# Kernel optimization log

Hardware: AMD Instinct MI355X
Metric: run time of the kernel (lower is better)

## Reference

```python
import jax, jax.numpy as jnp
import numpy as np

N = 50000   # nodes
E = 800000  # edges
B = 512     # graphs
EPS = 1e-5  # BatchNorm eps


def _p(k, shape, scale=0.05):
    return jax.random.normal(k, shape, dtype=jnp.float32) * scale


def setup_inputs() -> dict:
    key = jax.random.key(0)
    ks = jax.random.split(key, 24)
    inp = {
        "x": jax.random.normal(ks[0], (N, 4), dtype=jnp.float32),
        "edge_index": jax.random.randint(ks[1], (2, E), 0, N, dtype=jnp.int64),
        "edge_weight": jax.random.uniform(ks[2], (E,), dtype=jnp.float32),
        "batch": jnp.sort(jax.random.randint(ks[3], (N,), 0, B, dtype=jnp.int64)),
        # block1: GCNConv(4,64) + BN + shortcut Linear(4,64)
        "W1": _p(ks[4], (4, 64)), "b1": jnp.zeros((64,), jnp.float32),
        "g1": jnp.ones((64,), jnp.float32), "be1": jnp.zeros((64,), jnp.float32),
        "sW1": _p(ks[5], (4, 64)), "sb1": jnp.zeros((64,), jnp.float32),
        # block2: GCNConv(64,64) + BN, identity shortcut
        "W2": _p(ks[6], (64, 64)), "b2": jnp.zeros((64,), jnp.float32),
        "g2": jnp.ones((64,), jnp.float32), "be2": jnp.zeros((64,), jnp.float32),
        # block3: GCNConv(64,128) + BN + shortcut Linear(64,128)
        "W3": _p(ks[7], (64, 128)), "b3": jnp.zeros((128,), jnp.float32),
        "g3": jnp.ones((128,), jnp.float32), "be3": jnp.zeros((128,), jnp.float32),
        "sW3": _p(ks[8], (64, 128)), "sb3": jnp.zeros((128,), jnp.float32),
        # head: Linear(256,128) + BN + ReLU + Linear(128,1)
        "fW1": _p(ks[9], (256, 128)), "fb1": jnp.zeros((128,), jnp.float32),
        "fg": jnp.ones((128,), jnp.float32), "fbe": jnp.zeros((128,), jnp.float32),
        "fW2": _p(ks[10], (128, 1)), "fb2": jnp.zeros((1,), jnp.float32),
    }
    return inp


def _bn(x, g, b):
    # training-mode BatchNorm1d over node dim (biased variance)
    m = x.mean(0)
    v = x.var(0)
    return (x - m) * jax.lax.rsqrt(v + EPS) * g + b


def _gcn(x, W, b, src, dst, w, n):
    # PyG GCNConv: add self-loops (weight 1), symmetric normalization
    h = x @ W  # [n, out]
    loop = jnp.arange(n)
    s = jnp.concatenate([src, loop])
    d = jnp.concatenate([dst, loop])
    ww = jnp.concatenate([w, jnp.ones((n,), x.dtype)])
    deg = jax.ops.segment_sum(ww, d, num_segments=n)
    dis = jnp.where(deg > 0, jax.lax.rsqrt(jnp.maximum(deg, EPS)), 0.0)
    norm = dis[s] * ww * dis[d]  # [E+n]
    return jax.ops.segment_sum(h[s] * norm[:, None], d, num_segments=n) + b


def _block(x, W, b, g, be, sW, sb, src, dst, w, n):
    out = jax.nn.relu(_bn(_gcn(x, W, b, src, dst, w, n), g, be))
    sc = x if sW is None else x @ sW + sb
    return out + sc


def reference(x, edge_index, edge_weight, batch,
              W1, b1, g1, be1, sW1, sb1,
              W2, b2, g2, be2,
              W3, b3, g3, be3, sW3, sb3,
              fW1, fb1, fg, fbe, fW2, fb2):
    n = x.shape[0]
    src, dst = edge_index[0], edge_index[1]
    h = _block(x, W1, b1, g1, be1, sW1, sb1, src, dst, edge_weight, n)
    h = _block(h, W2, b2, g2, be2, None, None, src, dst, edge_weight, n)
    h = _block(h, W3, b3, g3, be3, sW3, sb3, src, dst, edge_weight, n)
    # global mean / max pooling per graph
    cnt = jax.ops.segment_sum(jnp.ones((n,), h.dtype), batch, num_segments=B)
    p1 = jax.ops.segment_sum(h, batch, num_segments=B) / jnp.maximum(cnt, 1.0)[:, None]
    p2 = jax.ops.segment_max(h, batch, num_segments=B)
    z = jnp.concatenate([p1, p2], axis=1)  # [B, 256]
    z = jax.nn.relu(_bn(z @ fW1 + fb1, fg, fbe))  # Dropout eval = identity
    return z @ fW2 + fb2  # [B, 1]
```

## Files before the change

### kernel.cpp

```cpp
#include <hip/hip_runtime.h>

#define BNEPS 1e-5f


__global__ void k_fill(float* p, int n, float v){
  int i = blockIdx.x*blockDim.x + threadIdx.x;
  if(i < n) p[i] = v;
}


__global__ void k_count(int* cnt, const int* __restrict__ dst, int E){
  int e = blockIdx.x*blockDim.x + threadIdx.x;
  if(e < E) atomicAdd(&cnt[dst[e]], 1);
}

__global__ void k_scan1(int* cnt, int* rowptr, int* bsum, int n){
  __shared__ int sh[256];
  int tid = threadIdx.x;
  int i = blockIdx.x*256 + tid;
  int v = (i < n) ? cnt[i] : 0;
  sh[tid] = v;
  __syncthreads();
  for(int o = 1; o < 256; o <<= 1){
    int t = (tid >= o) ? sh[tid-o] : 0;
    __syncthreads();
    sh[tid] += t;
    __syncthreads();
  }
  if(i < n){ rowptr[i] = sh[tid] - v; cnt[i] = 0; }
  if(tid == 255) bsum[blockIdx.x] = sh[255];
}

__global__ void k_scan2(int* bsum, int m){
  __shared__ int sh[256];
  int tid = threadIdx.x;
  int v = (tid < m) ? bsum[tid] : 0;
  sh[tid] = v;
  __syncthreads();
  for(int o = 1; o < 256; o <<= 1){
    int t = (tid >= o) ? sh[tid-o] : 0;
    __syncthreads();
    sh[tid] += t;
    __syncthreads();
  }
  if(tid < m) bsum[tid] = sh[tid] - v;
}

__global__ void k_scan3(int* rowptr, const int* bsum, int n, int E){
  int i = blockIdx.x*blockDim.x + threadIdx.x;
  if(i < n) rowptr[i] += bsum[i >> 8];
  if(i == 0) rowptr[n] = E;
}

__global__ void k_scatter2(const int* __restrict__ src, const int* __restrict__ dst,
                           const float* __restrict__ w, const int* __restrict__ rowptr,
                           int* cur, int2* __restrict__ erec, int E){
  int e = blockIdx.x*blockDim.x + threadIdx.x;
  if(e >= E) return;
  int d = dst[e];
  int idx = rowptr[d] + atomicAdd(&cur[d], 1);
  erec[idx] = make_int2(src[e], __float_as_int(w[e]));
}

__global__ void k_degdis(const int2* __restrict__ erec, const int* __restrict__ rowptr,
                         float* __restrict__ dis, int n){
  int i = blockIdx.x*blockDim.x + threadIdx.x;
  if(i >= n) return;
  float s = 1.0f;
  int e0 = rowptr[i], e1 = rowptr[i+1];
  for(int j = e0; j < e1; j++) s += __int_as_float(erec[j].y);
  dis[i] = rsqrtf(s);
}

__global__ void k_mknorm(int2* __restrict__ erec, const int* __restrict__ rowptr,
                         const float* __restrict__ dis, int n){
  int i = blockIdx.x*blockDim.x + threadIdx.x;
  if(i >= n) return;
  float di = dis[i];
  int e0 = rowptr[i], e1 = rowptr[i+1];
  for(int j = e0; j < e1; j++){
    int2 r = erec[j];
    erec[j].y = __float_as_int(dis[r.x] * __int_as_float(r.y) * di);
  }
}


__global__ __launch_bounds__(256)
void k_gcn1_fused(const float* __restrict__ X, const float* __restrict__ dis,
                  const int* __restrict__ rowptr, const int2* __restrict__ erec,
                  const float* __restrict__ W, const float* __restrict__ bias,
                  float* __restrict__ H, float* __restrict__ stats, int n){
  const int tid = threadIdx.x;
  const int lane = tid & 63;
  const int wid = tid >> 6;
  const int eg = lane >> 2;
  const int ch = lane & 3;
  const float w0 = W[lane], w1 = W[64+lane], w2 = W[128+lane], w3 = W[192+lane];
  const float bc = bias[lane];
  float s = 0.f, s2 = 0.f;
  for(int i = blockIdx.x*4 + wid; i < n; i += gridDim.x*4){
    int e0 = rowptr[i], e1 = rowptr[i+1];
    float acc = 0.f;
    for(int j = e0 + eg; j < e1; j += 16){
      int2 r = erec[j];
      acc += X[(size_t)r.x*4 + ch] * __int_as_float(r.y);
    }
    if(eg == 0){
      float d = dis[i];
      acc += X[(size_t)i*4 + ch] * d * d;
    }
    acc += __shfl_xor(acc, 4);
    acc += __shfl_xor(acc, 8);
    acc += __shfl_xor(acc, 16);
    acc += __shfl_xor(acc, 32);
    float p0 = __shfl(acc, 0), p1 = __shfl(acc, 1);
    float p2 = __shfl(acc, 2), p3 = __shfl(acc, 3);
    float h = bc + p0*w0 + p1*w1 + p2*w2 + p3*w3;
    H[(size_t)i*64 + lane] = h;
    s += h; s2 += h*h;
  }
  __shared__ float rs[256], rs2[256];
  rs[tid] = s; rs2[tid] = s2;
  __syncthreads();
  if(tid < 64){
    atomicAdd(&stats[tid],    rs[tid]+rs[tid+64]+rs[tid+128]+rs[tid+192]);
    atomicAdd(&stats[64+tid], rs2[tid]+rs2[tid+64]+rs2[tid+128]+rs2[tid+192]);
  }
}


template<int C>
__global__ void k_gather(const float* __restrict__ H, const float* __restrict__ dis,
                         const int* __restrict__ rowptr, const int2* __restrict__ erec,
                         float* __restrict__ P, int n){
  const int NPB = 256 / C;
  int i = blockIdx.x*NPB + threadIdx.x / C;
  int c = threadIdx.x % C;
  if(i >= n) return;
  float di = dis[i];
  float acc = H[(size_t)i*C + c]*di*di;
  int e0 = rowptr[i], e1 = rowptr[i+1];
  int j = e0;
  for(; j + 8 <= e1; j += 8){
    int2 r0 = erec[j],   r1 = erec[j+1], r2 = erec[j+2], r3 = erec[j+3];
    int2 r4 = erec[j+4], r5 = erec[j+5], r6 = erec[j+6], r7 = erec[j+7];
    float h0 = H[(size_t)r0.x*C + c];
    float h1 = H[(size_t)r1.x*C + c];
    float h2 = H[(size_t)r2.x*C + c];
    float h3 = H[(size_t)r3.x*C + c];
    float h4 = H[(size_t)r4.x*C + c];
    float h5 = H[(size_t)r5.x*C + c];
    float h6 = H[(size_t)r6.x*C + c];
    float h7 = H[(size_t)r7.x*C + c];
    acc += h0*__int_as_float(r0.y) + h1*__int_as_float(r1.y)
         + h2*__int_as_float(r2.y) + h3*__int_as_float(r3.y)
         + h4*__int_as_float(r4.y) + h5*__int_as_float(r5.y)
         + h6*__int_as_float(r6.y) + h7*__int_as_float(r7.y);
  }
  for(; j < e1; j++){
    int2 r = erec[j];
    acc += H[(size_t)r.x*C + c] * __int_as_float(r.y);
  }
  P[(size_t)i*C + c] = acc;
}


template<int C>
__global__ __launch_bounds__(256)
void k_gemm_tile(const float* __restrict__ X, const float* __restrict__ W,
                 const float* __restrict__ bias, float* __restrict__ H,
                 float* __restrict__ stats, int n, int ntiles){
  const int RR = C/16;
  const int CG = C/4;
  __shared__ float Xs[64*65];
  __shared__ float Ws[64*C];
  __shared__ float sst[2*C];
  const int tid = threadIdx.x;
  const int cg = tid % CG, rg = tid / CG;
  const int c0 = cg*4;
  for(int t = tid; t < 16*C; t += 256)
    reinterpret_cast<float4*>(Ws)[t] = reinterpret_cast<const float4*>(W)[t];
  const float4 bc = *reinterpret_cast<const float4*>(bias + c0);
  float sacc[4] = {0,0,0,0}, qacc[4] = {0,0,0,0};
  const float4* X4 = reinterpret_cast<const float4*>(X);
  for(int tile = blockIdx.x; tile < ntiles; tile += gridDim.x){
    const int r0 = tile*64;
    __syncthreads();
    #pragma unroll
    for(int q = 0; q < 4; q++){
      int idx = tid + q*256;
      int row = idx >> 4, k4 = idx & 15;
      float4 v = (r0+row < n) ? X4[(size_t)(r0+row)*16 + k4] : make_float4(0.f,0.f,0.f,0.f);
      Xs[(4*k4+0)*65 + row] = v.x;
      Xs[(4*k4+1)*65 + row] = v.y;
      Xs[(4*k4+2)*65 + row] = v.z;
      Xs[(4*k4+3)*65 + row] = v.w;
    }
    __syncthreads();
    float acc[RR][4];
    #pragma unroll
    for(int r = 0; r < RR; r++){ acc[r][0]=bc.x; acc[r][1]=bc.y; acc[r][2]=bc.z; acc[r][3]=bc.w; }
    #pragma unroll 8
    for(int k = 0; k < 64; k++){
      float4 wv = reinterpret_cast<const float4*>(Ws)[k*CG + cg];
      #pragma unroll
      for(int r = 0; r < RR; r++){
        float xv = Xs[k*65 + rg*RR + r];
        acc[r][0] = fmaf(xv, wv.x, acc[r][0]);
        acc[r][1] = fmaf(xv, wv.y, acc[r][1]);
        acc[r][2] = fmaf(xv, wv.z, acc[r][2]);
        acc[r][3] = fmaf(xv, wv.w, acc[r][3]);
      }
    }
    #pragma unroll
    for(int r = 0; r < RR; r++){
      int row = r0 + rg*RR + r;
      if(row < n){
        *reinterpret_cast<float4*>(H + (size_t)row*C + c0) =
            make_float4(acc[r][0], acc[r][1], acc[r][2], acc[r][3]);
        #pragma unroll
        for(int j = 0; j < 4; j++){ sacc[j] += acc[r][j]; qacc[j] += acc[r][j]*acc[r][j]; }
      }
    }
  }
  for(int t = tid; t < 2*C; t += 256) sst[t] = 0.f;
  __syncthreads();
  #pragma unroll
  for(int j = 0; j < 4; j++){
    atomicAdd(&sst[c0+j], sacc[j]);
    atomicAdd(&sst[C+c0+j], qacc[j]);
  }
  __syncthreads();
  for(int t = tid; t < 2*C; t += 256) atomicAdd(&stats[t], sst[t]);
}

template<int C>
__global__ __launch_bounds__(256)
void k_gemm_bnsc_tile(const float* __restrict__ X, const float* __restrict__ sW,
                      const float* __restrict__ sb,
                      const float* __restrict__ agg, const float* __restrict__ stats,
                      const float* __restrict__ g, const float* __restrict__ be,
                      float* __restrict__ out, int n, int ntiles){
  const int RR = C/16;
  const int CG = C/4;
  __shared__ float Xs[64*65];
  __shared__ float Ws[64*C];
  const int tid = threadIdx.x;
  const int cg = tid % CG, rg = tid / CG;
  const int c0 = cg*4;
  for(int t = tid; t < 16*C; t += 256)
    reinterpret_cast<float4*>(Ws)[t] = reinterpret_cast<const float4*>(sW)[t];
  const float4 bc = *reinterpret_cast<const float4*>(sb + c0);
  float scal[4], shft[4];
  {
    float invn = 1.0f / n;
    #pragma unroll
    for(int j = 0; j < 4; j++){
      float m = stats[c0+j]*invn;
      float v = stats[C+c0+j]*invn - m*m;
      float rs = rsqrtf(v + BNEPS) * g[c0+j];
      scal[j] = rs;
      shft[j] = be[c0+j] - m*rs;
    }
  }
  const float4* X4 = reinterpret_cast<const float4*>(X);
  for(int tile = blockIdx.x; tile < ntiles; tile += gridDim.x){
    const int r0 = tile*64;
    __syncthreads();
    #pragma unroll
    for(int q = 0; q < 4; q++){
      int idx = tid + q*256;
      int row = idx >> 4, k4 = idx & 15;
      float4 v = (r0+row < n) ? X4[(size_t)(r0+row)*16 + k4] : make_float4(0.f,0.f,0.f,0.f);
      Xs[(4*k4+0)*65 + row] = v.x;
      Xs[(4*k4+1)*65 + row] = v.y;
      Xs[(4*k4+2)*65 + row] = v.z;
      Xs[(4*k4+3)*65 + row] = v.w;
    }
    __syncthreads();
    float acc[RR][4];
    #pragma unroll
    for(int r = 0; r < RR; r++){ acc[r][0]=bc.x; acc[r][1]=bc.y; acc[r][2]=bc.z; acc[r][3]=bc.w; }
    #pragma unroll 8
    for(int k = 0; k < 64; k++){
      float4 wv = reinterpret_cast<const float4*>(Ws)[k*CG + cg];
      #pragma unroll
      for(int r = 0; r < RR; r++){
        float xv = Xs[k*65 + rg*RR + r];
        acc[r][0] = fmaf(xv, wv.x, acc[r][0]);
        acc[r][1] = fmaf(xv, wv.y, acc[r][1]);
        acc[r][2] = fmaf(xv, wv.z, acc[r][2]);
        acc[r][3] = fmaf(xv, wv.w, acc[r][3]);
      }
    }
    #pragma unroll
    for(int r = 0; r < RR; r++){
      int row = r0 + rg*RR + r;
      if(row < n){
        float4 a = *reinterpret_cast<const float4*>(agg + (size_t)row*C + c0);
        float4 o;
        o.x = fmaxf(a.x*scal[0] + shft[0], 0.f) + acc[r][0];
        o.y = fmaxf(a.y*scal[1] + shft[1], 0.f) + acc[r][1];
        o.z = fmaxf(a.z*scal[2] + shft[2], 0.f) + acc[r][2];
        o.w = fmaxf(a.w*scal[3] + shft[3], 0.f) + acc[r][3];
        *reinterpret_cast<float4*>(out + (size_t)row*C + c0) = o;
      }
    }
  }
}


template<int C>
__global__ void k_bn_add4(const float* __restrict__ agg, const float* __restrict__ stats,
                          const float* __restrict__ g, const float* __restrict__ be,
                          const float* __restrict__ add, float* __restrict__ out, int n){
  int idx = blockIdx.x*blockDim.x + threadIdx.x;
  if(idx >= n*(C/4)) return;
  int c = (idx % (C/4))*4;
  float invn = 1.0f / n;
  float4 sm = *reinterpret_cast<const float4*>(stats + c);
  float4 sq = *reinterpret_cast<const float4*>(stats + C + c);
  float4 g4 = *reinterpret_cast<const float4*>(g + c);
  float4 b4 = *reinterpret_cast<const float4*>(be + c);
  float4 a  = reinterpret_cast<const float4*>(agg)[idx];
  float4 ad = reinterpret_cast<const float4*>(add)[idx];
  float4 o;
  #define BN1(X) { float m = sm.X*invn; float v = sq.X*invn - m*m; \
    o.X = fmaxf((a.X-m)*rsqrtf(v+BNEPS)*g4.X + b4.X, 0.f) + ad.X; }
  BN1(x) BN1(y) BN1(z) BN1(w)
  #undef BN1
  reinterpret_cast<float4*>(out)[idx] = o;
}

__global__ void k_bn_sc4_v4(const float* __restrict__ agg, const float* __restrict__ stats,
                            const float* __restrict__ g, const float* __restrict__ be,
                            const float* __restrict__ X, const float* __restrict__ sW,
                            const float* __restrict__ sb, float* __restrict__ out, int n){
  int idx = blockIdx.x*blockDim.x + threadIdx.x;
  if(idx >= n*16) return;
  int i = idx >> 4;
  int c = (idx & 15)*4;
  float invn = 1.0f / n;
  float4 xr = *reinterpret_cast<const float4*>(X + (size_t)i*4);
  float4 s0 = *reinterpret_cast<const float4*>(sW + c);
  float4 s1 = *reinterpret_cast<const float4*>(sW + 64 + c);
  float4 s2 = *reinterpret_cast<const float4*>(sW + 128 + c);
  float4 s3 = *reinterpret_cast<const float4*>(sW + 192 + c);
  float4 sb4 = *reinterpret_cast<const float4*>(sb + c);
  float4 sm = *reinterpret_cast<const float4*>(stats + c);
  float4 sq = *reinterpret_cast<const float4*>(stats + 64 + c);
  float4 g4 = *reinterpret_cast<const float4*>(g + c);
  float4 b4 = *reinterpret_cast<const float4*>(be + c);
  float4 a  = reinterpret_cast<const float4*>(agg)[idx];
  float4 o;
  #define BN1(X) { float sc = xr.x*s0.X + xr.y*s1.X + xr.z*s2.X + xr.w*s3.X + sb4.X; \
    float m = sm.X*invn; float v = sq.X*invn - m*m; \
    o.X = fmaxf((a.X-m)*rsqrtf(v+BNEPS)*g4.X + b4.X, 0.f) + sc; }
  BN1(x) BN1(y) BN1(z) BN1(w)
  #undef BN1
  reinterpret_cast<float4*>(out)[idx] = o;
}


__global__ void k_pool(const float* __restrict__ H, const int* __restrict__ batch,
                       float* __restrict__ z, int n){
  int b = blockIdx.x, c = threadIdx.x;
  int lo = 0, hi = n;
  while(lo < hi){ int mid = (lo+hi)>>1; if(batch[mid] <  b) lo = mid+1; else hi = mid; }
  int start = lo;
  hi = n;
  while(lo < hi){ int mid = (lo+hi)>>1; if(batch[mid] <  b+1) lo = mid+1; else hi = mid; }
  int end = lo;
  float s = 0.f, mx = -INFINITY;
  for(int i = start; i < end; i++){
    float v = H[(size_t)i*128 + c];
    s += v; mx = fmaxf(mx, v);
  }
  int cnt = end - start;
  z[b*256 + c]       = s / fmaxf((float)cnt, 1.f);
  z[b*256 + 128 + c] = mx;
}

__global__ void k_head1(const float* __restrict__ z, const float* __restrict__ fW1,
                        const float* __restrict__ fb1, float* __restrict__ zr,
                        float* __restrict__ stats, int B){
  int idx = blockIdx.x*blockDim.x + threadIdx.x;
  int tid = threadIdx.x;
  float acc = 0.f;
  if(idx < B*128){
    int b = idx >> 7, c = idx & 127;
    acc = fb1[c];
    #pragma unroll 4
    for(int k = 0; k < 256; k++) acc = fmaf(z[b*256+k], fW1[k*128+c], acc);
    zr[idx] = acc;
  }
  __shared__ float rs[256], rs2[256];
  rs[tid] = acc; rs2[tid] = acc*acc;
  __syncthreads();
  if(tid < 128){
    atomicAdd(&stats[tid],     rs[tid]+rs[tid+128]);
    atomicAdd(&stats[128+tid], rs2[tid]+rs2[tid+128]);
  }
}

__global__ void k_final(const float* __restrict__ zr, const float* __restrict__ stats,
                        const float* __restrict__ fg, const float* __restrict__ fbe,
                        const float* __restrict__ fW2, const float* __restrict__ fb2,
                        float* __restrict__ out, int B){
  __shared__ float red[128];
  int b = blockIdx.x, c = threadIdx.x;
  float invn = 1.0f / B;
  float m  = stats[c]*invn;
  float v  = stats[128+c]*invn - m*m;
  float rs = rsqrtf(v + BNEPS);
  float val = fmaxf((zr[b*128+c]-m)*rs*fg[c] + fbe[c], 0.f) * fW2[c];
  red[c] = val;
  __syncthreads();
  for(int s = 64; s > 0; s >>= 1){
    if(c < s) red[c] += red[c+s];
    __syncthreads();
  }
  if(c == 0) out[b] = red[0] + fb2[0];
}


extern "C" void kernel_launch(void* const* d_in, const int* in_sizes, int n_in,
                              void* d_out, int out_size, void* d_ws, size_t ws_size,
                              hipStream_t stream){
  const float* x   = (const float*)d_in[0];
  const int*   ei  = (const int*)  d_in[1];
  const float* ew  = (const float*)d_in[2];
  const int*   bat = (const int*)  d_in[3];
  const float* W1  = (const float*)d_in[4];  const float* b1  = (const float*)d_in[5];
  const float* g1  = (const float*)d_in[6];  const float* be1 = (const float*)d_in[7];
  const float* sW1 = (const float*)d_in[8];  const float* sb1 = (const float*)d_in[9];
  const float* W2  = (const float*)d_in[10]; const float* b2  = (const float*)d_in[11];
  const float* g2  = (const float*)d_in[12]; const float* be2 = (const float*)d_in[13];
  const float* W3  = (const float*)d_in[14]; const float* b3  = (const float*)d_in[15];
  const float* g3  = (const float*)d_in[16]; const float* be3 = (const float*)d_in[17];
  const float* sW3 = (const float*)d_in[18]; const float* sb3 = (const float*)d_in[19];
  const float* fW1 = (const float*)d_in[20]; const float* fb1 = (const float*)d_in[21];
  const float* fg  = (const float*)d_in[22]; const float* fbe = (const float*)d_in[23];
  const float* fW2 = (const float*)d_in[24]; const float* fb2 = (const float*)d_in[25];
  float* out = (float*)d_out;

  const int n = in_sizes[0] / 4;
  const int E = in_sizes[2];
  const int B = out_size;
  const int* src = ei;
  const int* dst = ei + E;

  auto GB = [](long long t){ return (int)((t + 255) / 256); };
  const int nscanb = (n + 255) / 256;
  const int ntiles = (n + 63) / 64;

  float* ws = (float*)d_ws;
  size_t off = 0;
  auto alloc = [&](size_t cnt)->float*{ float* p = ws + off; off += (cnt + 63) & ~size_t(63); return p; };

  const size_t npad = ((size_t)n + 63) & ~size_t(63);
  float* bufA  = alloc((size_t)n * 64);
  float* hbuf  = alloc((size_t)n * 128);
  float* agg   = alloc((size_t)n * 128);
  float* z     = alloc((size_t)B * 256);
  float* zr    = alloc((size_t)B * 128);
  float* zreg  = alloc(npad + 1024);
  int*   cnt   = (int*)zreg;
  float* st1 = zreg + npad; float* st2 = st1 + 256;
  float* st3 = st2 + 256;   float* stH = st3 + 256;
  float* dis    = alloc(n);
  int*   rowptr = (int*)alloc(n + 1);
  int*   bsum   = (int*)alloc(256);
  int2*  erec   = (int2*)alloc((size_t)E * 2);

  k_fill<<<GB(npad + 1024),256,0,stream>>>(zreg, (int)(npad + 1024), 0.f);
  k_count<<<GB(E),256,0,stream>>>(cnt, dst, E);
  k_scan1<<<nscanb,256,0,stream>>>(cnt, rowptr, bsum, n);
  k_scan2<<<1,256,0,stream>>>(bsum, nscanb);
  k_scan3<<<GB(n),256,0,stream>>>(rowptr, bsum, n, E);
  k_scatter2<<<GB(E),256,0,stream>>>(src, dst, ew, rowptr, cnt, erec, E);
  k_degdis<<<GB(n),256,0,stream>>>(erec, rowptr, dis, n);
  k_mknorm<<<GB(n),256,0,stream>>>(erec, rowptr, dis, n);

  float* P = hbuf;
  k_gcn1_fused<<<512,256,0,stream>>>(x, dis, rowptr, erec, W1, b1, agg, st1, n);
  k_bn_sc4_v4<<<GB((long long)n*16),256,0,stream>>>(agg, st1, g1, be1, x, sW1, sb1, bufA, n);

  k_gather<64><<<(n+3)/4,256,0,stream>>>(bufA, dis, rowptr, erec, P, n);
  k_gemm_tile<64><<<512,256,0,stream>>>(P, W2, b2, agg, st2, n, ntiles);
  k_bn_add4<64><<<GB((long long)n*16),256,0,stream>>>(agg, st2, g2, be2, bufA, bufA, n);

  k_gather<64><<<(n+3)/4,256,0,stream>>>(bufA, dis, rowptr, erec, P, n);
  k_gemm_tile<128><<<512,256,0,stream>>>(P, W3, b3, agg, st3, n, ntiles);
  k_gemm_bnsc_tile<128><<<512,256,0,stream>>>(bufA, sW3, sb3, agg, st3, g3, be3, hbuf, n, ntiles);

  k_pool<<<B,128,0,stream>>>(hbuf, bat, z, n);
  k_head1<<<GB((long long)B*128),256,0,stream>>>(z, fW1, fb1, zr, stH, B);
  k_final<<<B,128,0,stream>>>(zr, stH, fg, fbe, fW2, fb2, out, B);
}
```

Measured before the change: 487.5 us.

## Store 64-wide node features in fp16 and reuse atomic ranks for CSR scatter

The 64-channel intermediate feature buffer is now stored as half precision, and the gather, BN-add, BN-shortcut and shortcut-GEMM kernels read and write it as fp16. Arithmetic stays in fp32. This halves the bytes moved in the random-access neighbour gathers and the elementwise passes, at the cost of rounding the residual activations to fp16. Separately, the count kernel now records each edge's atomic rank so the scatter no longer needs a second round of atomics, which costs an extra E-sized buffer. The first fused GCN kernel also gets a larger grid.

After: 468.8 us. -3.8%, faster.

```diff
diff --git a/kernel.cpp b/kernel.cpp
--- a/kernel.cpp
+++ b/kernel.cpp
@@ -1,4 +1,5 @@
 #include <hip/hip_runtime.h>
+#include <hip/hip_fp16.h>
 
 #define BNEPS 1e-5f
 
@@ -9,12 +10,12 @@
 }
 
 
-__global__ void k_count(int* cnt, const int* __restrict__ dst, int E){
+__global__ void k_count(int* cnt, int* rank, const int* __restrict__ dst, int E){
   int e = blockIdx.x*blockDim.x + threadIdx.x;
-  if(e < E) atomicAdd(&cnt[dst[e]], 1);
-}
-
-__global__ void k_scan1(int* cnt, int* rowptr, int* bsum, int n){
+  if(e < E) rank[e] = atomicAdd(&cnt[dst[e]], 1);
+}
+
+__global__ void k_scan1(const int* __restrict__ cnt, int* rowptr, int* bsum, int n){
   __shared__ int sh[256];
   int tid = threadIdx.x;
   int i = blockIdx.x*256 + tid;
@@ -27,7 +28,7 @@
     sh[tid] += t;
     __syncthreads();
   }
-  if(i < n){ rowptr[i] = sh[tid] - v; cnt[i] = 0; }
+  if(i < n) rowptr[i] = sh[tid] - v;
   if(tid == 255) bsum[blockIdx.x] = sh[255];
 }
 
@@ -54,12 +55,11 @@
 
 __global__ void k_scatter2(const int* __restrict__ src, const int* __restrict__ dst,
                            const float* __restrict__ w, const int* __restrict__ rowptr,
-                           int* cur, int2* __restrict__ erec, int E){
+                           const int* __restrict__ rank, int2* __restrict__ erec, int E){
   int e = blockIdx.x*blockDim.x + threadIdx.x;
   if(e >= E) return;
   int d = dst[e];
-  int idx = rowptr[d] + atomicAdd(&cur[d], 1);
-  erec[idx] = make_int2(src[e], __float_as_int(w[e]));
+  erec[rowptr[d] + rank[e]] = make_int2(src[e], __float_as_int(w[e]));
 }
 
 __global__ void k_degdis(const int2* __restrict__ erec, const int* __restrict__ rowptr,
@@ -129,29 +129,27 @@
 }
 
 
-template<int C>
-__global__ void k_gather(const float* __restrict__ H, const float* __restrict__ dis,
-                         const int* __restrict__ rowptr, const int2* __restrict__ erec,
-                         float* __restrict__ P, int n){
-  const int NPB = 256 / C;
-  int i = blockIdx.x*NPB + threadIdx.x / C;
-  int c = threadIdx.x % C;
+__global__ void k_gather64h(const __half* __restrict__ H, const float* __restrict__ dis,
+                            const int* __restrict__ rowptr, const int2* __restrict__ erec,
+                            float* __restrict__ P, int n){
+  int i = blockIdx.x*4 + threadIdx.x / 64;
+  int c = threadIdx.x & 63;
   if(i >= n) return;
   float di = dis[i];
-  float acc = H[(size_t)i*C + c]*di*di;
+  float acc = __half2float(H[(size_t)i*64 + c])*di*di;
   int e0 = rowptr[i], e1 = rowptr[i+1];
   int j = e0;
   for(; j + 8 <= e1; j += 8){
     int2 r0 = erec[j],   r1 = erec[j+1], r2 = erec[j+2], r3 = erec[j+3];
     int2 r4 = erec[j+4], r5 = erec[j+5], r6 = erec[j+6], r7 = erec[j+7];
-    float h0 = H[(size_t)r0.x*C + c];
-    float h1 = H[(size_t)r1.x*C + c];
-    float h2 = H[(size_t)r2.x*C + c];
-    float h3 = H[(size_t)r3.x*C + c];
-    float h4 = H[(size_t)r4.x*C + c];
-    float h5 = H[(size_t)r5.x*C + c];
-    float h6 = H[(size_t)r6.x*C + c];
-    float h7 = H[(size_t)r7.x*C + c];
+    float h0 = __half2float(H[(size_t)r0.x*64 + c]);
+    float h1 = __half2float(H[(size_t)r1.x*64 + c]);
+    float h2 = __half2float(H[(size_t)r2.x*64 + c]);
+    float h3 = __half2float(H[(size_t)r3.x*64 + c]);
+    float h4 = __half2float(H[(size_t)r4.x*64 + c]);
+    float h5 = __half2float(H[(size_t)r5.x*64 + c]);
+    float h6 = __half2float(H[(size_t)r6.x*64 + c]);
+    float h7 = __half2float(H[(size_t)r7.x*64 + c]);
     acc += h0*__int_as_float(r0.y) + h1*__int_as_float(r1.y)
          + h2*__int_as_float(r2.y) + h3*__int_as_float(r3.y)
          + h4*__int_as_float(r4.y) + h5*__int_as_float(r5.y)
@@ -159,9 +157,9 @@
   }
   for(; j < e1; j++){
     int2 r = erec[j];
-    acc += H[(size_t)r.x*C + c] * __int_as_float(r.y);
-  }
-  P[(size_t)i*C + c] = acc;
+    acc += __half2float(H[(size_t)r.x*64 + c]) * __int_as_float(r.y);
+  }
+  P[(size_t)i*64 + c] = acc;
 }
 
 
@@ -234,15 +232,13 @@
   for(int t = tid; t < 2*C; t += 256) atomicAdd(&stats[t], sst[t]);
 }
 
-template<int C>
 __global__ __launch_bounds__(256)
-void k_gemm_bnsc_tile(const float* __restrict__ X, const float* __restrict__ sW,
-                      const float* __restrict__ sb,
-                      const float* __restrict__ agg, const float* __restrict__ stats,
-                      const float* __restrict__ g, const float* __restrict__ be,
-                      float* __restrict__ out, int n, int ntiles){
-  const int RR = C/16;
-  const int CG = C/4;
+void k_gemm_bnsc_tile_h(const __half* __restrict__ Xh, const float* __restrict__ sW,
+                        const float* __restrict__ sb,
+                        const float* __restrict__ agg, const float* __restrict__ stats,
+                        const float* __restrict__ g, const float* __restrict__ be,
+                        float* __restrict__ out, int n, int ntiles){
+  const int C = 128, RR = 8, CG = 32;
   __shared__ float Xs[64*65];
   __shared__ float Ws[64*C];
   const int tid = threadIdx.x;
@@ -263,19 +259,22 @@
       shft[j] = be[c0+j] - m*rs;
     }
   }
-  const float4* X4 = reinterpret_cast<const float4*>(X);
   for(int tile = blockIdx.x; tile < ntiles; tile += gridDim.x){
     const int r0 = tile*64;
     __syncthreads();
     #pragma unroll
-    for(int q = 0; q < 4; q++){
-      int idx = tid + q*256;
-      int row = idx >> 4, k4 = idx & 15;
-      float4 v = (r0+row < n) ? X4[(size_t)(r0+row)*16 + k4] : make_float4(0.f,0.f,0.f,0.f);
-      Xs[(4*k4+0)*65 + row] = v.x;
-      Xs[(4*k4+1)*65 + row] = v.y;
-      Xs[(4*k4+2)*65 + row] = v.z;
-      Xs[(4*k4+3)*65 + row] = v.w;
+    for(int q = 0; q < 2; q++){
+      int t = tid + q*256;
+      int row = t >> 3, h8 = t & 7;
+      float4 raw = make_float4(0.f,0.f,0.f,0.f);
+      if(r0+row < n) raw = *reinterpret_cast<const float4*>(Xh + (size_t)(r0+row)*64 + h8*8);
+      const __half2* hp = reinterpret_cast<const __half2*>(&raw);
+      #pragma unroll
+      for(int p = 0; p < 4; p++){
+        float2 f = __half22float2(hp[p]);
+        Xs[(h8*8 + 2*p    )*65 + row] = f.x;
+        Xs[(h8*8 + 2*p + 1)*65 + row] = f.y;
+      }
     }
     __syncthreads();
     float acc[RR][4];
@@ -310,32 +309,34 @@
 }
 
 
-template<int C>
-__global__ void k_bn_add4(const float* __restrict__ agg, const float* __restrict__ stats,
-                          const float* __restrict__ g, const float* __restrict__ be,
-                          const float* __restrict__ add, float* __restrict__ out, int n){
+__global__ void k_bn_add4_h(const float* __restrict__ agg, const float* __restrict__ stats,
+                            const float* __restrict__ g, const float* __restrict__ be,
+                            __half* __restrict__ buf, int n){
   int idx = blockIdx.x*blockDim.x + threadIdx.x;
-  if(idx >= n*(C/4)) return;
-  int c = (idx % (C/4))*4;
+  if(idx >= n*16) return;
+  int c = (idx & 15)*4;
   float invn = 1.0f / n;
   float4 sm = *reinterpret_cast<const float4*>(stats + c);
-  float4 sq = *reinterpret_cast<const float4*>(stats + C + c);
+  float4 sq = *reinterpret_cast<const float4*>(stats + 64 + c);
   float4 g4 = *reinterpret_cast<const float4*>(g + c);
   float4 b4 = *reinterpret_cast<const float4*>(be + c);
   float4 a  = reinterpret_cast<const float4*>(agg)[idx];
-  float4 ad = reinterpret_cast<const float4*>(add)[idx];
-  float4 o;
-  #define BN1(X) { float m = sm.X*invn; float v = sq.X*invn - m*m; \
-    o.X = fmaxf((a.X-m)*rsqrtf(v+BNEPS)*g4.X + b4.X, 0.f) + ad.X; }
-  BN1(x) BN1(y) BN1(z) BN1(w)
-  #undef BN1
-  reinterpret_cast<float4*>(out)[idx] = o;
-}
-
-__global__ void k_bn_sc4_v4(const float* __restrict__ agg, const float* __restrict__ stats,
-                            const float* __restrict__ g, const float* __restrict__ be,
-                            const float* __restrict__ X, const float* __restrict__ sW,
-                            const float* __restrict__ sb, float* __restrict__ out, int n){
+  __half2* bp = reinterpret_cast<__half2*>(buf) + idx*2;
+  float2 ad01 = __half22float2(bp[0]);
+  float2 ad23 = __half22float2(bp[1]);
+  float o0,o1,o2,o3;
+  { float m=sm.x*invn, v=sq.x*invn-m*m; o0 = fmaxf((a.x-m)*rsqrtf(v+BNEPS)*g4.x+b4.x,0.f)+ad01.x; }
+  { float m=sm.y*invn, v=sq.y*invn-m*m; o1 = fmaxf((a.y-m)*rsqrtf(v+BNEPS)*g4.y+b4.y,0.f)+ad01.y; }
+  { float m=sm.z*invn, v=sq.z*invn-m*m; o2 = fmaxf((a.z-m)*rsqrtf(v+BNEPS)*g4.z+b4.z,0.f)+ad23.x; }
+  { float m=sm.w*invn, v=sq.w*invn-m*m; o3 = fmaxf((a.w-m)*rsqrtf(v+BNEPS)*g4.w+b4.w,0.f)+ad23.y; }
+  bp[0] = __floats2half2_rn(o0,o1);
+  bp[1] = __floats2half2_rn(o2,o3);
+}
+
+__global__ void k_bn_sc4_h(const float* __restrict__ agg, const float* __restrict__ stats,
+                           const float* __restrict__ g, const float* __restrict__ be,
+                           const float* __restrict__ X, const float* __restrict__ sW,
+                           const float* __restrict__ sb, __half* __restrict__ out, int n){
   int idx = blockIdx.x*blockDim.x + threadIdx.x;
   if(idx >= n*16) return;
   int i = idx >> 4;
@@ -352,13 +353,15 @@
   float4 g4 = *reinterpret_cast<const float4*>(g + c);
   float4 b4 = *reinterpret_cast<const float4*>(be + c);
   float4 a  = reinterpret_cast<const float4*>(agg)[idx];
-  float4 o;
-  #define BN1(X) { float sc = xr.x*s0.X + xr.y*s1.X + xr.z*s2.X + xr.w*s3.X + sb4.X; \
-    float m = sm.X*invn; float v = sq.X*invn - m*m; \
-    o.X = fmaxf((a.X-m)*rsqrtf(v+BNEPS)*g4.X + b4.X, 0.f) + sc; }
-  BN1(x) BN1(y) BN1(z) BN1(w)
+  float o0,o1,o2,o3;
+  #define BN1(X_, O_) { float sc = xr.x*s0.X_ + xr.y*s1.X_ + xr.z*s2.X_ + xr.w*s3.X_ + sb4.X_; \
+    float m = sm.X_*invn; float v = sq.X_*invn - m*m; \
+    O_ = fmaxf((a.X_-m)*rsqrtf(v+BNEPS)*g4.X_ + b4.X_, 0.f) + sc; }
+  BN1(x,o0) BN1(y,o1) BN1(z,o2) BN1(w,o3)
   #undef BN1
-  reinterpret_cast<float4*>(out)[idx] = o;
+  __half2* op = reinterpret_cast<__half2*>(out) + idx*2;
+  op[0] = __floats2half2_rn(o0,o1);
+  op[1] = __floats2half2_rn(o2,o3);
 }
 
 
@@ -459,7 +462,7 @@
   auto alloc = [&](size_t cnt)->float*{ float* p = ws + off; off += (cnt + 63) & ~size_t(63); return p; };
 
   const size_t npad = ((size_t)n + 63) & ~size_t(63);
-  float* bufA  = alloc((size_t)n * 64);
+  __half* bufA = (__half*)alloc((size_t)n * 32);
   float* hbuf  = alloc((size_t)n * 128);
   float* agg   = alloc((size_t)n * 128);
   float* z     = alloc((size_t)B * 256);
@@ -471,28 +474,29 @@
   float* dis    = alloc(n);
   int*   rowptr = (int*)alloc(n + 1);
   int*   bsum   = (int*)alloc(256);
+  int*   rank   = (int*)alloc(E);
   int2*  erec   = (int2*)alloc((size_t)E * 2);
 
   k_fill<<<GB(npad + 1024),256,0,stream>>>(zreg, (int)(npad + 1024), 0.f);
-  k_count<<<GB(E),256,0,stream>>>(cnt, dst, E);
+  k_count<<<GB(E),256,0,stream>>>(cnt, rank, dst, E);
   k_scan1<<<nscanb,256,0,stream>>>(cnt, rowptr, bsum, n);
   k_scan2<<<1,256,0,stream>>>(bsum, nscanb);
   k_scan3<<<GB(n),256,0,stream>>>(rowptr, bsum, n, E);
-  k_scatter2<<<GB(E),256,0,stream>>>(src, dst, ew, rowptr, cnt, erec, E);
+  k_scatter2<<<GB(E),256,0,stream>>>(src, dst, ew, rowptr, rank, erec, E);
   k_degdis<<<GB(n),256,0,stream>>>(erec, rowptr, dis, n);
   k_mknorm<<<GB(n),256,0,stream>>>(erec, rowptr, dis, n);
 
   float* P = hbuf;
-  k_gcn1_fused<<<512,256,0,stream>>>(x, dis, rowptr, erec, W1, b1, agg, st1, n);
-  k_bn_sc4_v4<<<GB((long long)n*16),256,0,stream>>>(agg, st1, g1, be1, x, sW1, sb1, bufA, n);
-
-  k_gather<64><<<(n+3)/4,256,0,stream>>>(bufA, dis, rowptr, erec, P, n);
+  k_gcn1_fused<<<2048,256,0,stream>>>(x, dis, rowptr, erec, W1, b1, agg, st1, n);
+  k_bn_sc4_h<<<GB((long long)n*16),256,0,stream>>>(agg, st1, g1, be1, x, sW1, sb1, bufA, n);
+
+  k_gather64h<<<(n+3)/4,256,0,stream>>>(bufA, dis, rowptr, erec, P, n);
   k_gemm_tile<64><<<512,256,0,stream>>>(P, W2, b2, agg, st2, n, ntiles);
-  k_bn_add4<64><<<GB((long long)n*16),256,0,stream>>>(agg, st2, g2, be2, bufA, bufA, n);
-
-  k_gather<64><<<(n+3)/4,256,0,stream>>>(bufA, dis, rowptr, erec, P, n);
+  k_bn_add4_h<<<GB((long long)n*16),256,0,stream>>>(agg, st2, g2, be2, bufA, n);
+
+  k_gather64h<<<(n+3)/4,256,0,stream>>>(bufA, dis, rowptr, erec, P, n);
   k_gemm_tile<128><<<512,256,0,stream>>>(P, W3, b3, agg, st3, n, ntiles);
-  k_gemm_bnsc_tile<128><<<512,256,0,stream>>>(bufA, sW3, sb3, agg, st3, g3, be3, hbuf, n, ntiles);
+  k_gemm_bnsc_tile_h<<<512,256,0,stream>>>(bufA, sW3, sb3, agg, st3, g3, be3, hbuf, n, ntiles);
 
   k_pool<<<B,128,0,stream>>>(hbuf, bat, z, n);
   k_head1<<<GB((long long)B*128),256,0,stream>>>(z, fW1, fb1, zr, stH, B);
```
